# Performance work log

Hardware: AMD Instinct MI355X
Metric: run time of the kernel (lower is better)

## Reference

```python
import jax, jax.numpy as jnp
import numpy as np
from jax import lax

F32 = jnp.float32
EDT_ITERS = 16  # iterations for erosion-based distance transform approximation


def _maxpool(x, win):
    # x: (B, 1, D, H, W); stride-1 'SAME' max pool (pads with -inf like torch)
    return lax.reduce_window(x, -jnp.inf, lax.max, (1, 1) + win, (1, 1, 1, 1, 1), 'SAME')


def _minpool(x, win):
    return -_maxpool(-x, win)


def soft_erode(img):
    p1 = _minpool(img, (3, 1, 1))
    p2 = _minpool(img, (1, 3, 1))
    p3 = _minpool(img, (1, 1, 3))
    return jnp.minimum(jnp.minimum(p1, p2), p3)


def soft_dilate(img):
    return _maxpool(img, (3, 3, 3))


def soft_open(img):
    return soft_dilate(soft_erode(img))


def soft_skel(img, num_iter=10):
    # clDice soft skeletonization (SoftSkeletonize, num_iter=10)
    skel = jax.nn.relu(img - soft_open(img))
    for _ in range(num_iter):
        img = soft_erode(img)
        delta = jax.nn.relu(img - soft_open(img))
        skel = skel + jax.nn.relu(delta - skel * delta)
    return skel


def edt_approx(mask):
    # mask: (B, D, H, W) binary float. Distance-to-background via iterated
    # 3x3x3 erosion (chessboard metric approximation of distance_transform_edt).
    m = mask[:, None]

    def body(carry, _):
        cur, acc = carry
        acc = acc + cur
        cur = _minpool(cur, (3, 3, 3))
        return (cur, acc), None

    (_, acc), _ = lax.scan(body, (m, jnp.zeros_like(m)), None, length=EDT_ITERS)
    return acc[:, 0]


def get_weights(mask_input, skel_input, prob_flag):
    # dim == 3 path of the original get_weights, vectorized over batch
    if prob_flag:
        mask = (mask_input > 0.5).astype(F32)
        skel = (skel_input > 0.5).astype(F32)
    else:
        mask, skel = mask_input, skel_input
    dist = lax.stop_gradient(edt_approx(mask)) * mask
    skel_radius = dist * skel
    red = (1, 2, 3)
    rmax = jnp.maximum(jnp.max(skel_radius, axis=red, keepdims=True), 1.0)
    rmin = jnp.maximum(jnp.min(skel_radius, axis=red, keepdims=True), 1.0)
    dist_map_norm = jnp.minimum(dist, rmax) / rmax
    skel_R_norm = skel_radius / rmax
    I_norm = ((rmax - skel_radius + rmin) / rmax) ** 2 * skel  # dim == 3 -> squared
    if prob_flag:
        return dist_map_norm * mask_input, skel_R_norm * mask_input, I_norm * skel_input
    return dist_map_norm * mask, skel_R_norm * mask, I_norm * skel


def binary_fg_prob(net_output):
    # max over foreground channels, 2-way softmax, foreground probability
    fore = jnp.max(net_output[:, 1:], axis=1, keepdims=True)
    logits2 = jnp.concatenate([net_output[:, :1], fore], axis=1)
    return jax.nn.softmax(logits2, axis=1)[:, 1]  # (B, D, H, W)


def general_union(pred, tgt, weight):
    smooth, alpha, eps = 1.0, 0.1, 1e-4
    inter = jnp.sum(weight * (pred + eps) ** 0.7 * tgt)
    union = jnp.sum(weight * (alpha * pred + (1.0 - alpha) * tgt))
    return 1.0 - (inter + smooth) / (union + smooth)


def union_loss(net_output, target):
    prob = binary_fg_prob(net_output)
    y_true = (target[:, 0] > 0).astype(F32)
    hard = lax.stop_gradient((prob > 0.5).astype(F32))
    skel_pred_hard = lax.stop_gradient(soft_skel(hard[:, None], 10)[:, 0])
    skel_true = lax.stop_gradient(soft_skel(y_true[:, None], 10)[:, 0])
    skel_pred_prob = skel_pred_hard * prob
    q_vl, _, q_sl = get_weights(y_true, skel_true, prob_flag=False)
    q_vp, _, q_sp = get_weights(prob, skel_pred_prob, prob_flag=True)
    return general_union(q_sp, q_vl, q_sp) + general_union(q_vp, q_sl, q_sl)


def cldice_loss(net_output, target, num_iter=10, smooth=1.0):
    prob = binary_fg_prob(net_output)
    y_true = (target[:, 0] > 0).astype(F32)
    skel_pred = soft_skel(prob[:, None], num_iter)[:, 0]
    skel_true = soft_skel(y_true[:, None], num_iter)[:, 0]
    tprec = (jnp.sum(skel_pred * y_true) + smooth) / (jnp.sum(skel_pred) + smooth)
    tsens = (jnp.sum(skel_true * prob) + smooth) / (jnp.sum(skel_true) + smooth)
    return 1.0 - 2.0 * tprec * tsens / (tprec + tsens)


def soft_dice_loss(net_output, target, smooth=1e-5):
    # nnUNet SoftDiceLoss: softmax nonlin, batch_dice=True, do_bg=False
    pred = jax.nn.softmax(net_output, axis=1)
    C = net_output.shape[1]
    onehot = jnp.moveaxis(jax.nn.one_hot(target[:, 0], C, dtype=F32), -1, 1)
    axes = (0, 2, 3, 4)
    tp = jnp.sum(pred * onehot, axis=axes)
    fp = jnp.sum(pred * (1.0 - onehot), axis=axes)
    fn = jnp.sum((1.0 - pred) * onehot, axis=axes)
    dc = (2.0 * tp + smooth) / (2.0 * tp + fp + fn + smooth)
    return -jnp.mean(dc[1:])


def ce_loss(net_output, labels):
    logp = jax.nn.log_softmax(net_output, axis=1)
    nll = -jnp.take_along_axis(logp, labels[:, None], axis=1)[:, 0]
    return jnp.mean(nll)


def _sobel_kernels():
    sx = np.array([[-1, 0, 1], [-2, 0, 2], [-1, 0, 1]], np.float32)
    kx_t = np.stack([sx, sx, sx], axis=0)[None, None]  # (1,1,3,3,3) OIDHW
    ky_t = np.transpose(kx_t, (0, 1, 3, 2, 4))
    kz_t = np.transpose(kx_t, (0, 1, 4, 2, 3))

    def pred_k(k):  # (1,2,3,3,3): second input channel is all-zero like the torch kernel
        return np.concatenate([k, np.zeros_like(k)], axis=1)

    return (pred_k(kx_t), pred_k(ky_t), pred_k(kz_t)), (kx_t, ky_t, kz_t)


def _conv3d(x, k):
    return lax.conv_general_dilated(x, jnp.asarray(k), (1, 1, 1), 'SAME',
                                    dimension_numbers=('NCDHW', 'OIDHW', 'NCDHW'))


def directional_loss(pred, target):
    kp, kt = _sobel_kernels()
    gp = jnp.stack([_conv3d(pred, k) for k in kp], axis=-1)    # (B,1,D,H,W,3)
    gt = jnp.stack([_conv3d(target, k) for k in kt], axis=-1)  # (B,1,D,H,W,3)

    def normalize(v):
        n = jnp.linalg.norm(v, axis=-1, keepdims=True)
        return v / jnp.maximum(n, 1e-12)

    gpn, gtn = normalize(gp), normalize(gt)
    num = jnp.sum(gpn * gtn, axis=-1)
    den = jnp.maximum(jnp.linalg.norm(gpn, axis=-1) * jnp.linalg.norm(gtn, axis=-1), 1e-8)
    return 1.0 - jnp.mean(num / den)


def connectivity_loss(pred, target):
    pb = (pred > 0.5).astype(F32)
    tb = (target > 0.5).astype(F32)
    return jnp.mean(jnp.abs(pb - tb))  # broadcasts (B,2,...) against (B,1,...)


def combined_loss(net_output, target):
    tgt_f = target.astype(F32)
    labels = target[:, 0]
    return (soft_dice_loss(net_output, target)
            + ce_loss(net_output, labels)
            + cldice_loss(net_output, target)
            + directional_loss(net_output, tgt_f)
            + connectivity_loss(net_output, tgt_f)
            + union_loss(net_output, target))


def setup_inputs() -> dict:
    key = jax.random.key(0)
    k1, k2 = jax.random.split(key)
    net_output = jax.random.normal(k1, (2, 2, 64, 128, 128), dtype=jnp.float32)
    target = jax.random.randint(k2, (2, 1, 64, 128, 128), 0, 2, dtype=jnp.int32)
    return {'net_output': net_output, 'target': target, 't_skeletonize_flage': 0}


def reference(net_output, target, t_skeletonize_flage):
    # t_skeletonize_flage=0 -> soft (morphological) skeletonization path
    return combined_loss(net_output, target)
```

## Files before the change

kernel.cpp:

```cpp
#include <hip/hip_runtime.h>
#include <math.h>

typedef unsigned long long u64;
typedef unsigned int u32;
typedef unsigned short u16;
typedef unsigned char u8;

#define VOL 1048576
#define NTOT 2097152
#define NWORDS 32768
#define PC0 2048
#define PC1 2048

union HU { u16 u; _Float16 h; };
__device__ __forceinline__ float h2f(u16 u){ HU x; x.u=u; return (float)x.h; }
__device__ __forceinline__ u16 f2h(float f){ HU x; x.h=(_Float16)f; return x.u; }
#define H_ONE2 0x3C003C00u

__device__ __forceinline__ u32 pmin(u32 a, u32 b){ u32 r; asm("v_pk_min_f16 %0, %1, %2" : "=v"(r) : "v"(a), "v"(b)); return r; }
__device__ __forceinline__ u32 pmax(u32 a, u32 b){ u32 r; asm("v_pk_max_f16 %0, %1, %2" : "=v"(r) : "v"(a), "v"(b)); return r; }

__device__ __forceinline__ double wred(double v){
  #pragma unroll
  for(int o=32;o;o>>=1) v += __shfl_down(v, o);
  return v;
}

__device__ __forceinline__ u32 nib_compact(u64 v){
  v &= 0x0F0F0F0F0F0F0F0Full;
  v |= v>>4;  v &= 0x00FF00FF00FF00FFull;
  v |= v>>8;  v &= 0x0000FFFF0000FFFFull;
  v |= v>>16;
  return (u32)v;
}

__global__ __launch_bounds__(256) void k_init(const float* __restrict__ net, const int* __restrict__ tgt,
    u16* __restrict__ img, u16* __restrict__ prob, u64* __restrict__ ybits, u64* __restrict__ hbits,
    u64* __restrict__ bimg2, double* __restrict__ part)
{
  __shared__ u64 nyb[32], nhb[32];
  __shared__ double sw[5][4];
  int tid = threadIdx.x;
  int r = blockIdx.x*256 + tid;
  int n0 = r<<2;
  int b = n0>>20, v0 = n0&(VOL-1);
  const float* nb = net + (size_t)b*(2*VOL);
  float4 a0 = *(const float4*)&nb[v0];
  float4 a1 = *(const float4*)&nb[VOL+v0];
  int4  tv = *(const int4*)&tgt[n0];
  float x0a[4] = {a0.x,a0.y,a0.z,a0.w};
  float x1a[4] = {a1.x,a1.y,a1.z,a1.w};
  int   ta[4]  = {tv.x,tv.y,tv.z,tv.w};
  double ce=0,tp=0,spr=0,sy=0,conn=0;
  u32 pk[2] = {0,0};
  u32 y4=0, h4=0;
  #pragma unroll
  for(int e=0;e<4;e++){
    float d = x1a[e]-x0a[e];
    int yb = (ta[e]>0) ? 1 : 0;
    float p = 1.f/(1.f+__expf(-d));
    y4 |= (u32)yb<<e;
    h4 |= (u32)(d>0.f)<<e;
    pk[e>>1] |= (u32)f2h(p) << ((e&1)*16);
    ce += (double)(log1pf(__expf(-fabsf(d))) + fmaxf(yb? -d : d, 0.f));
    tp += (double)p*yb;
    spr += (double)p;
    sy += (double)yb;
    conn += (double)((int)((x0a[e]>0.5f)!=(yb!=0)) + (int)((x1a[e]>0.5f)!=(yb!=0)));
  }
  u32* f1 = (u32*)img;
  u32* f4 = (u32*)prob;
  int pi = r<<1;
  f1[pi] = pk[0]; f1[pi+1] = pk[1];
  f4[pi] = pk[0]; f4[pi+1] = pk[1];
  ((u8*)nyb)[tid] = (u8)y4;
  ((u8*)nhb)[tid] = (u8)h4;
  __syncthreads();
  if (tid < 16){
    u64 wy = (u64)nib_compact(nyb[tid*2]) | ((u64)nib_compact(nyb[tid*2+1])<<32);
    u64 wh = (u64)nib_compact(nhb[tid*2]) | ((u64)nib_compact(nhb[tid*2+1])<<32);
    int wi = blockIdx.x*16 + tid;
    ybits[wi]=wy; bimg2[wi]=wy;
    hbits[wi]=wh; bimg2[NWORDS+wi]=wh;
  }
  int wid = tid>>6, lane = tid&63;
  double vals[5] = {ce,tp,spr,sy,conn};
  #pragma unroll
  for(int s=0;s<5;s++){ double rr = wred(vals[s]); if(lane==0) sw[s][wid]=rr; }
  __syncthreads();
  if(tid==0){
    #pragma unroll
    for(int s=0;s<5;s++) part[(size_t)s*PC0 + blockIdx.x] = sw[s][0]+sw[s][1]+sw[s][2]+sw[s][3];
  }
}

template<bool INIT>
__global__ __launch_bounds__(256) void fskel2(const u16* __restrict__ imgin, u16* __restrict__ imgout,
                                              u16* __restrict__ skel)
{
  __shared__ u32 A_[2800];
  __shared__ u32 B_[1728];
  __shared__ u32 C_[1080];
  int bid = blockIdx.x;
  int xb = bid&3, yb=(bid>>2)&15, zb=(bid>>6)&15, b=bid>>10;
  int X0=xb*32, Y0=yb*8, Z0=zb*4;
  const u32* vin = (const u32*)(imgin + (size_t)b*VOL);
  u32* vout = (u32*)(imgout + (size_t)b*VOL);
  u32* skl = (u32*)(skel + (size_t)b*VOL);
  int tid = threadIdx.x;

  {
    int y0 = tid/20, x0 = tid - y0*20;
    int gy0 = Y0-3+y0, gx0 = X0-4+2*x0;
    bool ok0 = ((unsigned)gy0<128u) & ((unsigned)gx0<128u);
    int gb0 = (gy0<<6)+(gx0>>1);
    int t1 = tid+256; int y1 = t1/20, x1 = t1-y1*20;
    int gy1 = Y0-3+y1, gx1 = X0-4+2*x1;
    bool hv1 = tid<24;
    bool ok1 = ((unsigned)gy1<128u) & ((unsigned)gx1<128u);
    int gb1 = (gy1<<6)+(gx1>>1);
    #pragma unroll
    for(int z=0; z<10; ++z){
      int gz = Z0-3+z;
      bool zok = (unsigned)gz<64u;
      int zb2 = gz<<13;
      A_[z*280+tid] = (zok&ok0) ? vin[zb2+gb0] : H_ONE2;
      if (hv1) A_[z*280+t1] = (zok&ok1) ? vin[zb2+gb1] : H_ONE2;
    }
  }
  __syncthreads();
  if (tid < 216){
    int y = tid/18, px = tid - y*18;
    int gy = Y0-2+y;
    bool yok = (unsigned)gy<128u;
    bool xout = ((X0==0)&&(px==0)) || ((X0==96)&&(px==17));
    #pragma unroll
    for(int z=0; z<8; ++z){
      bool zok = (unsigned)(Z0-2+z)<64u;
      u32 v = H_ONE2;
      if (zok && yok && !xout){
        int c = (z+1)*280 + (y+1)*20 + (px+1);
        u32 C0=A_[c], L=A_[c-1], R=A_[c+1];
        u32 SL=(L>>16)|(C0<<16), SR=(C0>>16)|(R<<16);
        u32 m = pmin(pmin(SL,SR), C0);
        m = pmin(m, pmin(A_[c-20],A_[c+20]));
        v = pmin(m, pmin(A_[c-280],A_[c+280]));
      }
      B_[z*216+tid] = v;
    }
  }
  __syncthreads();
  if (tid < 180){
    int y = tid/18, px = tid - y*18;
    int gy = Y0-1+y;
    bool yok = (unsigned)gy<128u;
    bool xout = ((X0==0)&&(px==0)) || ((X0==96)&&(px==17));
    bool ctr = (px>=1)&&(px<=16)&&(y>=1)&&(y<=8);
    int pxm = (px>0)? px-1 : 0;
    int pxp = (px<17)? px+1 : 17;
    int gb = (gy<<6)+((X0-2+2*px)>>1);
    #pragma unroll
    for(int z=0; z<6; ++z){
      int gz = Z0-1+z;
      bool zok = (unsigned)gz<64u;
      u32 v = 0;
      if (zok && yok && !xout){
        int c = (z+1)*216 + (y+1)*18;
        u32 C0=B_[c+px], L=B_[c+pxm], R=B_[c+pxp];
        u32 SL=(L>>16)|(C0<<16), SR=(C0>>16)|(R<<16);
        u32 m = pmin(pmin(SL,SR), C0);
        m = pmin(m, pmin(B_[c+px-18],B_[c+px+18]));
        v = pmin(m, pmin(B_[c-216+px],B_[c+216+px]));
      }
      C_[z*180+tid] = v;
      if (ctr && z>=1 && z<=4)
        vout[(gz<<13)+gb] = v;
    }
  }
  int col = tid>>1, zh = tid&1;
  int oy = col>>4, opx = col&15;
  u32 ek0[2], ek1[2];
  #pragma unroll
  for(int j=0;j<2;j++){
    int z = zh*2+j;
    ek0[j] = A_[(z+3)*280+(oy+3)*20+(opx+2)];
    ek1[j] = B_[(z+2)*216+(oy+2)*18+(opx+1)];
  }
  __syncthreads();
  u32* X1 = A_; u32* X2 = A_ + 960;
  if (tid < 160){
    int y = tid>>4, px = tid&15;
    int px1 = px+1;
    int gy = Y0-1+y;
    bool yok = (unsigned)gy<128u;
    bool mlo = (X0==0)&&(px==0);
    bool mhi = (X0==96)&&(px==15);
    #pragma unroll
    for(int z=0; z<6; ++z){
      bool zok = (unsigned)(Z0-1+z)<64u;
      {
        int c = (z+1)*216 + (y+1)*18 + px1;
        u32 C0=B_[c], L=B_[c-1], R=B_[c+1];
        if (mlo) L = 0;
        if (mhi) R = 0;
        u32 SL=(L>>16)|(C0<<16), SR=(C0>>16)|(R<<16);
        u32 v = pmax(pmax(SL,SR), C0);
        X1[z*160+tid] = (zok&&yok) ? v : 0;
      }
      {
        int c = z*180 + y*18 + px1;
        u32 C0=C_[c], L=C_[c-1], R=C_[c+1];
        u32 SL=(L>>16)|(C0<<16), SR=(C0>>16)|(R<<16);
        X2[z*160+tid] = pmax(pmax(SL,SR), C0);
      }
    }
  }
  __syncthreads();
  u32* Y1 = B_; u32* Y2 = B_ + 768;
  {
    int arr = tid>>7, rem = tid&127;
    int y = rem>>4, px = rem&15;
    const u32* Xs = arr ? X2 : X1;
    u32* Ys = arr ? Y2 : Y1;
    #pragma unroll
    for(int z=0; z<6; ++z){
      int c = z*160 + y*16 + px;
      Ys[z*128 + rem] = pmax(pmax(Xs[c], Xs[c+16]), Xs[c+32]);
    }
  }
  __syncthreads();
  {
    int gx = X0 + 2*opx;
    #pragma unroll
    for(int j=0;j<2;j++){
      int z = zh*2+j;
      int gz = Z0+z;
      int c = z*128 + oy*16 + opx;
      u32 o1 = pmax(pmax(Y1[c], Y1[c+128]), Y1[c+256]);
      u32 o2 = pmax(pmax(Y2[c], Y2[c+128]), Y2[c+256]);
      u32 idx = (u32)((gz<<13) + ((Y0+oy)<<6) + (gx>>1));
      float d0l = fmaxf(h2f((u16)ek0[j]) - h2f((u16)o1), 0.f);
      float d0h = fmaxf(h2f((u16)(ek0[j]>>16)) - h2f((u16)(o1>>16)), 0.f);
      float d1l = fmaxf(h2f((u16)ek1[j]) - h2f((u16)o2), 0.f);
      float d1h = fmaxf(h2f((u16)(ek1[j]>>16)) - h2f((u16)(o2>>16)), 0.f);
      float sl_, sh_;
      if (INIT){ sl_ = d0l; sh_ = d0h; }
      else {
        u32 swv = skl[idx];
        sl_ = h2f((u16)swv); sh_ = h2f((u16)(swv>>16));
        sl_ += fmaxf(d0l - sl_*d0l, 0.f); sh_ += fmaxf(d0h - sh_*d0h, 0.f);
      }
      sl_ += fmaxf(d1l - sl_*d1l, 0.f); sh_ += fmaxf(d1h - sh_*d1h, 0.f);
      skl[idx] = (u32)f2h(sl_) | ((u32)f2h(sh_)<<16);
    }
  }
}

__global__ __launch_bounds__(256) void fskel1(const u16* __restrict__ imgin, u16* __restrict__ skel)
{
  __shared__ u32 A2[1920];
  __shared__ u32 B2[1080];
  int bid = blockIdx.x;
  int xb = bid&3, yb=(bid>>2)&15, zb=(bid>>6)&15, b=bid>>10;
  int X0=xb*32, Y0=yb*8, Z0=zb*4;
  const u32* vin = (const u32*)(imgin + (size_t)b*VOL);
  u32* skl = (u32*)(skel + (size_t)b*VOL);
  int tid = threadIdx.x;
  if (tid < 240){
    int y0 = tid/20, x0 = tid - y0*20;
    int gy0 = Y0-2+y0, gx0 = X0-4+2*x0;
    bool ok0 = ((unsigned)gy0<128u) & ((unsigned)gx0<128u);
    int gb0 = (gy0<<6)+(gx0>>1);
    #pragma unroll
    for(int z=0; z<8; ++z){
      int gz = Z0-2+z;
      bool zok = (unsigned)gz<64u;
      A2[z*240+tid] = (zok&ok0) ? vin[(gz<<13)+gb0] : H_ONE2;
    }
  }
  __syncthreads();
  if (tid < 180){
    int y = tid/18, px = tid - y*18;
    int gy = Y0-1+y;
    bool yok = (unsigned)gy<128u;
    bool xout = ((X0==0)&&(px==0)) || ((X0==96)&&(px==17));
    int pxm = (px>0)? px-1 : 0;
    int pxp = (px<17)? px+1 : 17;
    #pragma unroll
    for(int z=0; z<6; ++z){
      bool zok = (unsigned)(Z0-1+z)<64u;
      u32 v = 0;
      if (zok && yok && !xout){
        int c = (z+1)*240 + (y+1)*20;
        u32 C0=A2[c+px+1], L=A2[c+pxm+1], R=A2[c+pxp+1];
        u32 SL=(L>>16)|(C0<<16), SR=(C0>>16)|(R<<16);
        u32 m = pmin(pmin(SL,SR), C0);
        m = pmin(m, pmin(A2[c+px+1-20],A2[c+px+1+20]));
        v = pmin(m, pmin(A2[c-240+px+1],A2[c+240+px+1]));
      }
      B2[z*180+tid] = v;
    }
  }
  int col = tid>>1, zh = tid&1;
  int oy = col>>4, opx = col&15;
  u32 ek[2];
  #pragma unroll
  for(int j=0;j<2;j++){
    int z = zh*2+j;
    ek[j] = A2[(z+2)*240+(oy+2)*20+(opx+2)];
  }
  __syncthreads();
  u32* X = A2;
  if (tid < 160){
    int y = tid>>4, px = tid&15;
    int px1 = px+1;
    #pragma unroll
    for(int z=0; z<6; ++z){
      int c = z*180 + y*18 + px1;
      u32 C0=B2[c], L=B2[c-1], R=B2[c+1];
      u32 SL=(L>>16)|(C0<<16), SR=(C0>>16)|(R<<16);
      X[z*160+tid] = pmax(pmax(SL,SR), C0);
    }
  }
  __syncthreads();
  u32* Y = B2;
  if (tid < 128){
    int y = tid>>4, px = tid&15;
    #pragma unroll
    for(int z=0; z<6; ++z){
      int c = z*160 + y*16 + px;
      Y[z*128 + tid] = pmax(pmax(X[c], X[c+16]), X[c+32]);
    }
  }
  __syncthreads();
  {
    int gx = X0 + 2*opx;
    #pragma unroll
    for(int j=0;j<2;j++){
      int z = zh*2+j;
      int gz = Z0+z;
      int c = z*128 + oy*16 + opx;
      u32 o = pmax(pmax(Y[c], Y[c+128]), Y[c+256]);
      u32 idx = (u32)((gz<<13) + ((Y0+oy)<<6) + (gx>>1));
      float dl = fmaxf(h2f((u16)ek[j]) - h2f((u16)o), 0.f);
      float dh = fmaxf(h2f((u16)(ek[j]>>16)) - h2f((u16)(o>>16)), 0.f);
      u32 swv = skl[idx];
      float sl_ = h2f((u16)swv), sh_ = h2f((u16)(swv>>16));
      sl_ += fmaxf(dl - sl_*dl, 0.f); sh_ += fmaxf(dh - sh_*dh, 0.f);
      skl[idx] = (u32)f2h(sl_) | ((u32)f2h(sh_)<<16);
    }
  }
}

__device__ __forceinline__ u64 berode_x(const u64* P, int tid){
  u64 c = P[tid];
  if (tid & 1) return c & ((c<<1)|(P[tid-1]>>63)) & ((c>>1)|(1ull<<63));
  else         return c & ((c<<1)|1ull) & ((c>>1)|(P[tid+1]<<63));
}
__device__ __forceinline__ u64 bdilate_x(const u64* P, int tid){
  u64 c = P[tid];
  if (tid & 1) return c | (c<<1) | (P[tid-1]>>63) | (c>>1);
  else         return c | (c<<1) | (c>>1) | (P[tid+1]<<63);
}

template<bool INIT>
__global__ __launch_bounds__(256) void bskel(const u64* __restrict__ imgin, u64* __restrict__ imgout,
                                             u64* __restrict__ skel)
{
  __shared__ u64 simg[4][256];
  __shared__ u64 se1[6][256];
  __shared__ u64 se2[2][256];
  __shared__ u64 sM[4][256];
  int bid = blockIdx.x;
  int tzb = bid & 31, b = (bid>>5)&1, m = bid>>6;
  int z0 = tzb*2, z1 = z0+2;
  size_t base = (size_t)m*NWORDS + (size_t)b*16384;
  const u64* vin = imgin + base;
  u64* vout = imgout + base;
  u64* skl = skel + base;
  int tid = threadIdx.x;
  int y = tid>>1;

  for (int s = z0-3; s <= z1+6; ++s){
    if (s <= z1+2)
      simg[(s+96)&3][tid] = ((unsigned)s<64u) ? vin[(s<<8)+tid] : ~0ull;
    { int t = s-2;
      if (t >= z0-2 && t <= z1+1){
        u64 r = ~0ull;
        if ((unsigned)t<64u){
          const u64* P = simg[(t+96)&3];
          if (INIT) r = P[tid];
          else {
            r = berode_x(P, tid);
            if(y>0)   r &= P[tid-2];
            if(y<127) r &= P[tid+2];
            r &= simg[(t-1+96)&3][tid] & simg[(t+1+96)&3][tid];
          }
        }
        se1[(t+96)%6][tid] = r;
      }
    }
    { int t = s-4;
      if (t >= z0-1 && t <= z1){
        u64 r = 0;
        if ((unsigned)t<64u){
          const u64* P = se1[(t+96)%6];
          r = berode_x(P, tid);
          if(y>0)   r &= P[tid-2];
          if(y<127) r &= P[tid+2];
          r &= se1[(t-1+96)%6][tid] & se1[(t+1+96)%6][tid];
        }
        se2[(t+96)&1][tid] = r;
      }
    }
    { int t = s-5;
      if (t >= z0-1 && t <= z1){
        const u64* P = se2[(t+96)&1];
        u64 dm = bdilate_x(P, tid);
        if(y>0)   dm |= bdilate_x(P, tid-2);
        if(y<127) dm |= bdilate_x(P, tid+2);
        sM[(t+96)&3][tid] = dm;
      }
    }
    { int z = s-7;
      if (z >= z0 && z < z1){
        u64 open_ = sM[(z-1+96)&3][tid] | sM[(z+96)&3][tid] | sM[(z+1+96)&3][tid];
        u64 e1v = se1[(z+96)%6][tid];
        u64 d = e1v & ~open_;
        int gw = (z<<8)+tid;
        if (INIT) skl[gw] = d;
        else { skl[gw] |= d; vout[gw] = e1v; }
      }
    }
    __syncthreads();
  }
}

__global__ __launch_bounds__(256) void edt_px(const u64* __restrict__ yb, const u64* __restrict__ hb,
                                              u8* __restrict__ d)
{
  int g = blockIdx.x*256 + threadIdx.x;
  int m = g >> 21;
  int n = g & (NTOT-1);
  const u64* bits = m ? hb : yb;
  int x = n & 127;
  int row = n >> 7;
  u64 w0 = bits[row*2], w1 = bits[row*2+1];
  int a = x - 31;
  u64 win;
  if (a < 0)        win = w0 << (-a);
  else if (a == 0)  win = w0;
  else if (a < 64)  win = (w0 >> a) | (w1 << (64-a));
  else              win = w1 >> (a-64);
  if (x < 31)  win |= (1ull << (31-x)) - 1;
  if (x > 95)  win |= (~0ull) << (159-x);
  u64 inv = ~win;
  u64 tl = inv & 0xFFFFFFFFull;
  u64 tr = inv >> 31;
  int dl = tl ? (31 - (63 - __clzll(tl))) : 99;
  int dr = tr ? (__ffsll((unsigned long long)tr) - 1) : 99;
  d[(size_t)g] = (u8)min(min(dl, dr), 16);
}

__global__ __launch_bounds__(256) void edt_py(const u8* __restrict__ din, u8* __restrict__ dout){
  int g = blockIdx.x*256 + threadIdx.x;
  int n = g & (NTOT-1);
  int c = (n >> 7) & 127;
  size_t idx = (size_t)g;
  int best = din[idx];
  #pragma unroll 4
  for (int k=1; k<=16; ++k){
    if (best <= k) break;
    int v = 255;
    if (c-k >= 0)   v = din[idx - (size_t)k*128];
    if (c+k < 128)  v = min(v, (int)din[idx + (size_t)k*128]);
    best = min(best, max(k, v));
  }
  dout[idx] = (u8)best;
}

__global__ __launch_bounds__(256) void edt_pz_part(const u8* __restrict__ din, u8* __restrict__ dout,
    const u64* __restrict__ skel2, const u64* __restrict__ hbits,
    u8* __restrict__ pmaxv, u8* __restrict__ pminv)
{
  int tid = threadIdx.x;
  int g = blockIdx.x*256 + tid;
  int m = g >> 21;
  int n = g & (NTOT-1);
  int c = (n >> 14) & 63;
  size_t idx = (size_t)g;
  int best = din[idx];
  #pragma unroll 4
  for (int k=1; k<=16; ++k){
    if (best <= k) break;
    int v = 255;
    if (c-k >= 0)  v = din[idx - (size_t)k*16384];
    if (c+k < 64)  v = min(v, (int)din[idx + (size_t)k*16384]);
    best = min(best, max(k, v));
  }
  dout[idx] = (u8)best;
  int wi = n>>6, bit = n&63;
  u64 sbit = m ? (skel2[NWORDS+wi] & hbits[wi]) : skel2[wi];
  u32 r = (u32)((sbit>>bit)&1ull) ? (u32)best : 0u;
  __shared__ u32 sx[256], sn_[256];
  sx[tid]=r; sn_[tid]=r;
  __syncthreads();
  for(int s=128;s>0;s>>=1){
    if(tid<s){
      if(sx[tid+s]>sx[tid]) sx[tid]=sx[tid+s];
      if(sn_[tid+s]<sn_[tid]) sn_[tid]=sn_[tid+s];
    }
    __syncthreads();
  }
  if(tid==0){ pmaxv[blockIdx.x]=(u8)sx[0]; pminv[blockIdx.x]=(u8)sn_[0]; }
}

__global__ __launch_bounds__(256) void rmm2(const u8* __restrict__ pmaxv, const u8* __restrict__ pminv,
                                            u32* __restrict__ mm){
  __shared__ u8 smx[4][256], smn[4][256];
  int tid = threadIdx.x;
  u8 mx[4]={0,0,0,0}, mn[4]={255,255,255,255};
  for(int i=tid;i<16384;i+=256){
    int sel=i>>13, b=(i>>12)&1, cc=sel*2+b;
    u8 a=pmaxv[i], d=pminv[i];
    if(a>mx[cc]) mx[cc]=a;
    if(d<mn[cc]) mn[cc]=d;
  }
  #pragma unroll
  for(int cc=0;cc<4;cc++){ smx[cc][tid]=mx[cc]; smn[cc][tid]=mn[cc]; }
  __syncthreads();
  for(int s=128;s>0;s>>=1){
    if(tid<s){
      #pragma unroll
      for(int cc=0;cc<4;cc++){
        if(smx[cc][tid+s]>smx[cc][tid]) smx[cc][tid]=smx[cc][tid+s];
        if(smn[cc][tid+s]<smn[cc][tid]) smn[cc][tid]=smn[cc][tid+s];
      }
    }
    __syncthreads();
  }
  if(tid==0){
    #pragma unroll
    for(int cc=0;cc<4;cc++){
      int sel=cc>>1, b=cc&1;
      mm[sel*4+b]   = (u32)smx[cc][0];
      mm[sel*4+2+b] = (u32)smn[cc][0];
    }
  }
}

__global__ __launch_bounds__(256) void k_tail(const float* __restrict__ net, const u16* __restrict__ prob,
    const u16* __restrict__ skelp, const u64* __restrict__ ybits, const u64* __restrict__ hbits,
    const u64* __restrict__ skel2, const u8* __restrict__ acc, const u32* __restrict__ mm,
    double* __restrict__ part1)
{
  __shared__ float lp[2040];
  __shared__ float dxp[1920];
  __shared__ float sxp[1920];
  __shared__ char  dxt8[1920];
  __shared__ u8    sxt8[1920];
  __shared__ u64   wrow[60];
  __shared__ double sw[9][4];
  int tid = threadIdx.x;
  int bid = blockIdx.x;
  int xb = bid&3, ybk=(bid>>2)&15, zbk=(bid>>6)&15, b=bid>>10;
  int X0=xb*32, Y0=ybk*8, Z0=zbk*4;
  const float* P = net + (size_t)b*(2*VOL);
  float rmaxT = fmaxf((float)mm[b],1.f),   rminT = fmaxf((float)mm[2+b],1.f);
  float rmaxH = fmaxf((float)mm[4+b],1.f), rminH = fmaxf((float)mm[6+b],1.f);
  for (int idx=tid; idx<2040; idx+=256){
    int zr = idx/340; int rem = idx-zr*340; int yr = rem/34; int xi = rem-yr*34;
    int gz=Z0-1+zr, gy=Y0-1+yr, gx=X0-1+xi;
    float v = 0.f;
    if((unsigned)gz<64u && (unsigned)gy<128u && (unsigned)gx<128u)
      v = P[(gz<<14)+(gy<<7)+gx];
    lp[idx] = v;
  }
  if (tid < 60){
    int zr = tid/10, yr = tid-zr*10;
    int gz=Z0-1+zr, gy=Y0-1+yr;
    u64 wn = 0;
    if((unsigned)gz<64u && (unsigned)gy<128u){
      const u64* yw = ybits + ((size_t)b<<14) + (gz<<8) + (gy<<1);
      u64 w0 = yw[0], w1 = yw[1];
      if (X0==0) wn = w0<<1;
      else { int s = X0-1; wn = (s<64) ? ((w0>>s)|(w1<<(64-s))) : (w1>>(s-64)); }
    }
    wrow[tid] = wn;
  }
  __syncthreads();
  for (int idx=tid; idx<1920; idx+=256){
    int zr = idx/320; int rem = idx-zr*320; int yr = rem>>5; int x = rem&31;
    int c = zr*340 + yr*34 + x;
    float l0=lp[c], l1=lp[c+1], l2=lp[c+2];
    dxp[idx] = l2-l0;
    sxp[idx] = l0+2.f*l1+l2;
    u64 wn = wrow[zr*10+yr];
    int bm=(int)((wn>>x)&1ull), b1=(int)((wn>>(x+1))&1ull), bp=(int)((wn>>(x+2))&1ull);
    dxt8[idx] = (char)(bp-bm);
    sxt8[idx] = (u8)(bm+2*b1+bp);
  }
  __syncthreads();
  int oy = tid>>5, ox = tid&31;
  float A1[6],A2[6],A3[6];
  int   B1v[6],B2v[6],B3v[6];
  #pragma unroll
  for(int zr=0; zr<6; ++zr){
    int base = zr*320 + oy*32 + ox;
    float d0=dxp[base], d1=dxp[base+32], d2=dxp[base+64];
    A1[zr] = d0+2.f*d1+d2;
    A2[zr] = d0+d1+d2;
    float s0=sxp[base], s1=sxp[base+32], s2=sxp[base+64];
    A3[zr] = s0+s1+s2;
    int t0=dxt8[base], t1=dxt8[base+32], t2=dxt8[base+64];
    B1v[zr] = t0+2*t1+t2;
    B2v[zr] = t0+t1+t2;
    int u0=sxt8[base], u1=sxt8[base+32], u2=sxt8[base+64];
    B3v[zr] = u0+u1+u2;
  }
  double fsob=0,cl1=0,cl2=0,cl3=0,cl4=0,i1=0,un1=0,i2=0,un2=0;
  #pragma unroll
  for(int zc=0; zc<4; ++zc){
    float gpx = A1[zc]+A1[zc+1]+A1[zc+2];
    float gpy = A2[zc]+2.f*A2[zc+1]+A2[zc+2];
    float gpz = A3[zc+2]-A3[zc];
    float ftx = (float)(B1v[zc]+B1v[zc+1]+B1v[zc+2]);
    float fty = (float)(B2v[zc]+2*B2v[zc+1]+B2v[zc+2]);
    float ftz = (float)(B3v[zc+2]-B3v[zc]);
    float s1 = gpx*gpx+gpy*gpy+gpz*gpz;
    float s2 = ftx*ftx+fty*fty+ftz*ftz;
    if (s1>0.f && s2>0.f){
      float ip = rsqrtf(s1), it = rsqrtf(s2);
      fsob += (double)((gpx*ftx+gpy*fty+gpz*ftz)*ip*it);
    }
    int gz=Z0+zc, gy=Y0+oy, gx=X0+ox;
    int n = (b<<20)+(gz<<14)+(gy<<7)+gx;
    int yb = (int)((wrow[(zc+1)*10+(oy+1)] >> (ox+1)) & 1ull);
    int wi = n>>6, bit = n&63;
    int hd = (int)((hbits[wi]>>bit)&1ull);
    int sT = (int)((skel2[wi]>>bit)&1ull);
    int sH = (int)((skel2[NWORDS+wi]>>bit)&1ull);
    float dT = (float)acc[n];
    float dH = (float)acc[(size_t)NTOT+n];
    float p  = h2f(prob[n]);
    float sk = h2f(skelp[n]);
    cl1 += (double)(sk*(float)yb);
    cl2 += (double)sk;
    float q_vl = yb ? fminf(dT,rmaxT)/rmaxT : 0.f;
    if (sT){
      cl3 += (double)p; cl4 += 1.0;
      float t=(rmaxT-dT+rminT)/rmaxT; float q_sl=t*t;
      float q_vp = fminf(dH,rmaxH)/rmaxH*p;
      i2  += (double)(q_sl*__powf(q_vp+1e-4f,0.7f)*q_sl);
      un2 += (double)(q_sl*(0.1f*q_vp+0.9f*q_sl));
    }
    if (sH & hd){
      float t=(rmaxH-dH+rminH)/rmaxH; float q_sp=t*t*p;
      i1  += (double)(q_sp*__powf(q_sp+1e-4f,0.7f)*q_vl);
      un1 += (double)(q_sp*(0.1f*q_sp+0.9f*q_vl));
    }
  }
  int wid = tid>>6, lane = tid&63;
  double vals[9] = {fsob,cl1,cl2,cl3,cl4,i1,un1,i2,un2};
  #pragma unroll
  for(int s=0;s<9;s++){ double rr = wred(vals[s]); if(lane==0) sw[s][wid]=rr; }
  __syncthreads();
  if(tid==0){
    #pragma unroll
    for(int s=0;s<9;s++) part1[(size_t)s*PC1 + bid] = sw[s][0]+sw[s][1]+sw[s][2]+sw[s][3];
  }
}

__global__ __launch_bounds__(256) void k_reduce_mid(const double* __restrict__ part0,
                                                    const double* __restrict__ part1,
                                                    double* __restrict__ tot){
  int s = blockIdx.x;
  const double* src; int n;
  if (s < 5){ src = part0 + (size_t)s*PC0; n = PC0; }
  else      { src = part1 + (size_t)(s-5)*PC1; n = PC1; }
  double v=0;
  for(int i=threadIdx.x;i<n;i+=256) v += src[i];
  __shared__ double sd[256];
  sd[threadIdx.x]=v; __syncthreads();
  for(int k=128;k>0;k>>=1){ if((int)threadIdx.x<k) sd[threadIdx.x]+=sd[threadIdx.x+k]; __syncthreads(); }
  if(threadIdx.x==0) tot[s]=sd[0];
}

__global__ void k_fin(const double* __restrict__ tot, float* __restrict__ out){
  if(threadIdx.x==0 && blockIdx.x==0){
    const double N = (double)NTOT;
    double ce = tot[0]/N;
    double tp=tot[1], fp=tot[2]-tot[1], fn=tot[3]-tot[1];
    double dice = -((2.0*tp+1e-5)/(2.0*tp+fp+fn+1e-5));
    double conn = tot[4]/(2.0*N);
    double dir  = 1.0 - tot[5]/N;
    double tprec = (tot[6]+1.0)/(tot[7]+1.0);
    double tsens = (tot[8]+1.0)/(tot[9]+1.0);
    double cld = 1.0 - 2.0*tprec*tsens/(tprec+tsens);
    double u1 = 1.0 - (tot[10]+1.0)/(tot[11]+1.0);
    double u2 = 1.0 - (tot[12]+1.0)/(tot[13]+1.0);
    out[0] = (float)(dice+ce+cld+dir+conn+u1+u2);
  }
}

extern "C" void kernel_launch(void* const* d_in, const int* in_sizes, int n_in,
                              void* d_out, int out_size, void* d_ws, size_t ws_size,
                              hipStream_t stream)
{
  (void)in_sizes; (void)n_in; (void)out_size; (void)ws_size;
  const float* net = (const float*)d_in[0];
  const int*   tgt = (const int*)d_in[1];
  float* out = (float*)d_out;
  char* w = (char*)d_ws;
  const size_t MB = 1024*1024;
  u16* F1 = (u16*)(w + 0*MB);
  u16* F2 = (u16*)(w + 4*MB);
  u16* F3 = (u16*)(w + 8*MB);
  u16* F4 = (u16*)(w + 12*MB);
  u64* ybits = (u64*)(w + 16*MB);
  u64* hbits = ybits + NWORDS;
  u64* skel2 = hbits + NWORDS;
  u64* bping = skel2 + 2*NWORDS;
  u64* bpong = bping + 2*NWORDS;
  u8*  dA    = (u8*)(bpong + 2*NWORDS);
  u8*  dB    = dA + (size_t)2*NTOT;
  double* part0 = (double*)(dB + (size_t)2*NTOT);
  double* part1 = part0 + (size_t)5*PC0;
  double* tot   = part1 + (size_t)9*PC1;
  u8* pmaxv = (u8*)(tot + 16);
  u8* pminv = pmaxv + 16384;
  u32* mm  = (u32*)(pminv + 16384);

  k_init<<<PC0, 256, 0, stream>>>(net, tgt, F1, F4, ybits, hbits, bping, part0);

  bskel<true><<<128,256,0,stream>>>(bping, bpong, skel2);
  {
    u64* pi=bping; u64* po=bpong;
    for(int i=0;i<10;i++){ bskel<false><<<128,256,0,stream>>>(pi,po,skel2); u64* t=pi; pi=po; po=t; }
  }

  fskel2<true><<<2048,256,0,stream>>>(F1, F3, F2);
  fskel2<false><<<2048,256,0,stream>>>(F3, F1, F2);
  fskel2<false><<<2048,256,0,stream>>>(F1, F3, F2);
  fskel2<false><<<2048,256,0,stream>>>(F3, F1, F2);
  fskel2<false><<<2048,256,0,stream>>>(F1, F3, F2);
  fskel1<<<2048,256,0,stream>>>(F3, F2);

  const int GE = (2*NTOT)/256;
  edt_px<<<GE,256,0,stream>>>(ybits, hbits, dA);
  edt_py<<<GE,256,0,stream>>>(dA, dB);
  edt_pz_part<<<GE,256,0,stream>>>(dB, dA, skel2, hbits, pmaxv, pminv);
  rmm2<<<1,256,0,stream>>>(pmaxv, pminv, mm);

  k_tail<<<PC1,256,0,stream>>>(net, F4, F2, ybits, hbits, skel2, dA, mm, part1);
  k_reduce_mid<<<14,256,0,stream>>>(part0, part1, tot);
  k_fin<<<1,64,0,stream>>>(tot, out);
}
```

Measured before the change: 321.5 us.

## Fuse EDT x-pass into init, atomic min/max, and enlarge skeleton tiles

```diff
diff --git a/kernel.cpp b/kernel.cpp
--- a/kernel.cpp
+++ b/kernel.cpp
@@ -34,13 +34,33 @@
   return (u32)v;
 }
 
+__device__ __forceinline__ int edt_x1(u64 w0, u64 w1, int x){
+  int a = x-31;
+  u64 win;
+  if (a<0)        win = w0 << (-a);
+  else if (a==0)  win = w0;
+  else if (a<64)  win = (w0>>a)|(w1<<(64-a));
+  else            win = w1>>(a-64);
+  if (x<31) win |= (1ull<<(31-x))-1;
+  if (x>95) win |= (~0ull)<<(159-x);
+  u64 inv = ~win;
+  u64 tl = inv & 0xFFFFFFFFull;
+  u64 tr = inv>>31;
+  int dl = tl ? (31-(63-__clzll(tl))) : 99;
+  int dr = tr ? (__ffsll((unsigned long long)tr)-1) : 99;
+  return min(min(dl,dr),16);
+}
+
 __global__ __launch_bounds__(256) void k_init(const float* __restrict__ net, const int* __restrict__ tgt,
     u16* __restrict__ img, u16* __restrict__ prob, u64* __restrict__ ybits, u64* __restrict__ hbits,
-    u64* __restrict__ bimg2, double* __restrict__ part)
+    u64* __restrict__ bimg2, u8* __restrict__ dA, u32* __restrict__ mm, double* __restrict__ part)
 {
   __shared__ u64 nyb[32], nhb[32];
+  __shared__ u64 swy[16], swh[16];
   __shared__ double sw[5][4];
   int tid = threadIdx.x;
+  if (blockIdx.x==0 && tid<8)
+    mm[tid] = (tid==2||tid==3||tid==6||tid==7) ? 0xFFFFFFFFu : 0u;
   int r = blockIdx.x*256 + tid;
   int n0 = r<<2;
   int b = n0>>20, v0 = n0&(VOL-1);
@@ -82,6 +102,24 @@
     int wi = blockIdx.x*16 + tid;
     ybits[wi]=wy; bimg2[wi]=wy;
     hbits[wi]=wh; bimg2[NWORDS+wi]=wh;
+    swy[tid]=wy; swh[tid]=wh;
+  }
+  __syncthreads();
+  {
+    int ln = tid<<2;
+    int row = ln>>7;
+    int xq = ln&127;
+    int gn0 = blockIdx.x*1024 + ln;
+    u64 wy0 = swy[row*2], wy1 = swy[row*2+1];
+    u64 wh0 = swh[row*2], wh1 = swh[row*2+1];
+    u32 oy4=0, oh4=0;
+    #pragma unroll
+    for(int e=0;e<4;e++){
+      oy4 |= (u32)edt_x1(wy0,wy1,xq+e) << (8*e);
+      oh4 |= (u32)edt_x1(wh0,wh1,xq+e) << (8*e);
+    }
+    *(u32*)&dA[gn0] = oy4;
+    *(u32*)&dA[(size_t)NTOT+gn0] = oh4;
   }
   int wid = tid>>6, lane = tid&63;
   double vals[5] = {ce,tp,spr,sy,conn};
@@ -95,145 +133,113 @@
 }
 
 template<bool INIT>
-__global__ __launch_bounds__(256) void fskel2(const u16* __restrict__ imgin, u16* __restrict__ imgout,
+__global__ __launch_bounds__(512) void fskel2(const u16* __restrict__ imgin, u16* __restrict__ imgout,
                                               u16* __restrict__ skel)
 {
-  __shared__ u32 A_[2800];
-  __shared__ u32 B_[1728];
-  __shared__ u32 C_[1080];
+  __shared__ u32 A_[3920];
+  __shared__ u32 B_[2592];
+  __shared__ u32 C_[1800];
   int bid = blockIdx.x;
-  int xb = bid&3, yb=(bid>>2)&15, zb=(bid>>6)&15, b=bid>>10;
-  int X0=xb*32, Y0=yb*8, Z0=zb*4;
+  int xb = bid&3, yb=(bid>>2)&15, zb=(bid>>6)&7, b=bid>>9;
+  int X0=xb*32, Y0=yb*8, Z0=zb*8;
   const u32* vin = (const u32*)(imgin + (size_t)b*VOL);
   u32* vout = (u32*)(imgout + (size_t)b*VOL);
   u32* skl = (u32*)(skel + (size_t)b*VOL);
   int tid = threadIdx.x;
 
-  {
-    int y0 = tid/20, x0 = tid - y0*20;
-    int gy0 = Y0-3+y0, gx0 = X0-4+2*x0;
-    bool ok0 = ((unsigned)gy0<128u) & ((unsigned)gx0<128u);
-    int gb0 = (gy0<<6)+(gx0>>1);
-    int t1 = tid+256; int y1 = t1/20, x1 = t1-y1*20;
-    int gy1 = Y0-3+y1, gx1 = X0-4+2*x1;
-    bool hv1 = tid<24;
-    bool ok1 = ((unsigned)gy1<128u) & ((unsigned)gx1<128u);
-    int gb1 = (gy1<<6)+(gx1>>1);
-    #pragma unroll
-    for(int z=0; z<10; ++z){
-      int gz = Z0-3+z;
-      bool zok = (unsigned)gz<64u;
-      int zb2 = gz<<13;
-      A_[z*280+tid] = (zok&ok0) ? vin[zb2+gb0] : H_ONE2;
-      if (hv1) A_[z*280+t1] = (zok&ok1) ? vin[zb2+gb1] : H_ONE2;
-    }
-  }
-  __syncthreads();
-  if (tid < 216){
-    int y = tid/18, px = tid - y*18;
-    int gy = Y0-2+y;
-    bool yok = (unsigned)gy<128u;
+  for (int idx=tid; idx<3920; idx+=512){
+    int z = idx/280; int rem = idx - z*280; int y = rem/20; int px = rem - y*20;
+    int gz = Z0-3+z, gy = Y0-3+y, gx = X0-4+2*px;
+    bool ok = ((unsigned)gz<64u) & ((unsigned)gy<128u) & ((unsigned)gx<128u);
+    A_[idx] = ok ? vin[(gz<<13)+(gy<<6)+(gx>>1)] : H_ONE2;
+  }
+  __syncthreads();
+  for (int idx=tid; idx<2592; idx+=512){
+    int z = idx/216; int rem = idx - z*216; int y = rem/18; int px = rem - y*18;
+    int gz = Z0-2+z, gy = Y0-2+y;
+    bool zok = (unsigned)gz<64u, yok = (unsigned)gy<128u;
     bool xout = ((X0==0)&&(px==0)) || ((X0==96)&&(px==17));
-    #pragma unroll
-    for(int z=0; z<8; ++z){
-      bool zok = (unsigned)(Z0-2+z)<64u;
-      u32 v = H_ONE2;
-      if (zok && yok && !xout){
-        int c = (z+1)*280 + (y+1)*20 + (px+1);
-        u32 C0=A_[c], L=A_[c-1], R=A_[c+1];
-        u32 SL=(L>>16)|(C0<<16), SR=(C0>>16)|(R<<16);
-        u32 m = pmin(pmin(SL,SR), C0);
-        m = pmin(m, pmin(A_[c-20],A_[c+20]));
-        v = pmin(m, pmin(A_[c-280],A_[c+280]));
-      }
-      B_[z*216+tid] = v;
-    }
-  }
-  __syncthreads();
-  if (tid < 180){
-    int y = tid/18, px = tid - y*18;
-    int gy = Y0-1+y;
-    bool yok = (unsigned)gy<128u;
+    u32 v = H_ONE2;
+    if (zok && yok && !xout){
+      int c = (z+1)*280 + (y+1)*20 + (px+1);
+      u32 C0=A_[c], L=A_[c-1], R=A_[c+1];
+      u32 SL=(L>>16)|(C0<<16), SR=(C0>>16)|(R<<16);
+      u32 m = pmin(pmin(SL,SR), C0);
+      m = pmin(m, pmin(A_[c-20],A_[c+20]));
+      v = pmin(m, pmin(A_[c-280],A_[c+280]));
+    }
+    B_[idx] = v;
+  }
+  __syncthreads();
+  for (int idx=tid; idx<1800; idx+=512){
+    int z = idx/180; int rem = idx - z*180; int y = rem/18; int px = rem - y*18;
+    int gz = Z0-1+z, gy = Y0-1+y;
+    bool zok=(unsigned)gz<64u, yok=(unsigned)gy<128u;
     bool xout = ((X0==0)&&(px==0)) || ((X0==96)&&(px==17));
-    bool ctr = (px>=1)&&(px<=16)&&(y>=1)&&(y<=8);
-    int pxm = (px>0)? px-1 : 0;
-    int pxp = (px<17)? px+1 : 17;
-    int gb = (gy<<6)+((X0-2+2*px)>>1);
-    #pragma unroll
-    for(int z=0; z<6; ++z){
-      int gz = Z0-1+z;
-      bool zok = (unsigned)gz<64u;
-      u32 v = 0;
-      if (zok && yok && !xout){
-        int c = (z+1)*216 + (y+1)*18;
-        u32 C0=B_[c+px], L=B_[c+pxm], R=B_[c+pxp];
-        u32 SL=(L>>16)|(C0<<16), SR=(C0>>16)|(R<<16);
-        u32 m = pmin(pmin(SL,SR), C0);
-        m = pmin(m, pmin(B_[c+px-18],B_[c+px+18]));
-        v = pmin(m, pmin(B_[c-216+px],B_[c+216+px]));
-      }
-      C_[z*180+tid] = v;
-      if (ctr && z>=1 && z<=4)
-        vout[(gz<<13)+gb] = v;
-    }
-  }
-  int col = tid>>1, zh = tid&1;
-  int oy = col>>4, opx = col&15;
+    int pxm = (px>0)?px-1:0, pxp=(px<17)?px+1:17;
+    u32 v = 0;
+    if (zok && yok && !xout){
+      int c = (z+1)*216 + (y+1)*18;
+      u32 C0=B_[c+px], L=B_[c+pxm], R=B_[c+pxp];
+      u32 SL=(L>>16)|(C0<<16), SR=(C0>>16)|(R<<16);
+      u32 m = pmin(pmin(SL,SR), C0);
+      m = pmin(m, pmin(B_[c+px-18],B_[c+px+18]));
+      v = pmin(m, pmin(B_[c-216+px],B_[c+216+px]));
+    }
+    C_[idx] = v;
+    if (px>=1 && px<=16 && y>=1 && y<=8 && z>=1 && z<=8)
+      vout[(gz<<13)+(gy<<6)+((X0-2+2*px)>>1)] = v;
+  }
+  int zq = tid>>7, cc = tid&127;
+  int oy = cc>>4, opx = cc&15;
   u32 ek0[2], ek1[2];
   #pragma unroll
   for(int j=0;j<2;j++){
-    int z = zh*2+j;
-    ek0[j] = A_[(z+3)*280+(oy+3)*20+(opx+2)];
-    ek1[j] = B_[(z+2)*216+(oy+2)*18+(opx+1)];
-  }
-  __syncthreads();
-  u32* X1 = A_; u32* X2 = A_ + 960;
-  if (tid < 160){
-    int y = tid>>4, px = tid&15;
-    int px1 = px+1;
-    int gy = Y0-1+y;
-    bool yok = (unsigned)gy<128u;
-    bool mlo = (X0==0)&&(px==0);
-    bool mhi = (X0==96)&&(px==15);
-    #pragma unroll
-    for(int z=0; z<6; ++z){
-      bool zok = (unsigned)(Z0-1+z)<64u;
-      {
-        int c = (z+1)*216 + (y+1)*18 + px1;
-        u32 C0=B_[c], L=B_[c-1], R=B_[c+1];
-        if (mlo) L = 0;
-        if (mhi) R = 0;
-        u32 SL=(L>>16)|(C0<<16), SR=(C0>>16)|(R<<16);
-        u32 v = pmax(pmax(SL,SR), C0);
-        X1[z*160+tid] = (zok&&yok) ? v : 0;
-      }
-      {
-        int c = z*180 + y*18 + px1;
-        u32 C0=C_[c], L=C_[c-1], R=C_[c+1];
-        u32 SL=(L>>16)|(C0<<16), SR=(C0>>16)|(R<<16);
-        X2[z*160+tid] = pmax(pmax(SL,SR), C0);
-      }
-    }
-  }
-  __syncthreads();
-  u32* Y1 = B_; u32* Y2 = B_ + 768;
-  {
-    int arr = tid>>7, rem = tid&127;
-    int y = rem>>4, px = rem&15;
+    int z = zq*2+j;
+    ek0[j] = A_[(z+3)*280 + (oy+3)*20 + (opx+2)];
+    ek1[j] = B_[(z+2)*216 + (oy+2)*18 + (opx+1)];
+  }
+  __syncthreads();
+  u32* X1 = A_; u32* X2 = A_ + 1600;
+  for (int idx=tid; idx<3200; idx+=512){
+    int arr = (idx>=1600);
+    int r2 = arr ? idx-1600 : idx;
+    int z = r2/160; int rem = r2 - z*160; int y = rem>>4; int px = rem&15;
+    u32 v;
+    if (!arr){
+      int gz = Z0-1+z, gy = Y0-1+y;
+      bool ok = ((unsigned)gz<64u) && ((unsigned)gy<128u);
+      int c = (z+1)*216 + (y+1)*18 + (px+1);
+      u32 C0=B_[c], L=B_[c-1], R=B_[c+1];
+      if ((X0==0)&&(px==0)) L=0;
+      if ((X0==96)&&(px==15)) R=0;
+      u32 SL=(L>>16)|(C0<<16), SR=(C0>>16)|(R<<16);
+      v = pmax(pmax(SL,SR), C0);
+      if (!ok) v = 0;
+    } else {
+      int c = z*180 + y*18 + (px+1);
+      u32 C0=C_[c], L=C_[c-1], R=C_[c+1];
+      u32 SL=(L>>16)|(C0<<16), SR=(C0>>16)|(R<<16);
+      v = pmax(pmax(SL,SR), C0);
+    }
+    A_[idx] = v;
+  }
+  __syncthreads();
+  for (int idx=tid; idx<2560; idx+=512){
+    int arr = (idx>=1280);
+    int r2 = arr ? idx-1280 : idx;
+    int z = r2>>7; int rem = r2&127; int y = rem>>4; int px = rem&15;
     const u32* Xs = arr ? X2 : X1;
-    u32* Ys = arr ? Y2 : Y1;
-    #pragma unroll
-    for(int z=0; z<6; ++z){
-      int c = z*160 + y*16 + px;
-      Ys[z*128 + rem] = pmax(pmax(Xs[c], Xs[c+16]), Xs[c+32]);
-    }
-  }
-  __syncthreads();
+    int c = z*160 + y*16 + px;
+    B_[idx] = pmax(pmax(Xs[c], Xs[c+16]), Xs[c+32]);
+  }
+  __syncthreads();
+  u32* Y1 = B_; u32* Y2 = B_ + 1280;
   {
     int gx = X0 + 2*opx;
     #pragma unroll
     for(int j=0;j<2;j++){
-      int z = zh*2+j;
+      int z = zq*2+j;
       int gz = Z0+z;
       int c = z*128 + oy*16 + opx;
       u32 o1 = pmax(pmax(Y1[c], Y1[c+128]), Y1[c+256]);
@@ -256,88 +262,70 @@
   }
 }
 
-__global__ __launch_bounds__(256) void fskel1(const u16* __restrict__ imgin, u16* __restrict__ skel)
+__global__ __launch_bounds__(512) void fskel1(const u16* __restrict__ imgin, u16* __restrict__ skel)
 {
-  __shared__ u32 A2[1920];
-  __shared__ u32 B2[1080];
+  __shared__ u32 A2[2880];
+  __shared__ u32 B2[1800];
   int bid = blockIdx.x;
-  int xb = bid&3, yb=(bid>>2)&15, zb=(bid>>6)&15, b=bid>>10;
-  int X0=xb*32, Y0=yb*8, Z0=zb*4;
+  int xb = bid&3, yb=(bid>>2)&15, zb=(bid>>6)&7, b=bid>>9;
+  int X0=xb*32, Y0=yb*8, Z0=zb*8;
   const u32* vin = (const u32*)(imgin + (size_t)b*VOL);
   u32* skl = (u32*)(skel + (size_t)b*VOL);
   int tid = threadIdx.x;
-  if (tid < 240){
-    int y0 = tid/20, x0 = tid - y0*20;
-    int gy0 = Y0-2+y0, gx0 = X0-4+2*x0;
-    bool ok0 = ((unsigned)gy0<128u) & ((unsigned)gx0<128u);
-    int gb0 = (gy0<<6)+(gx0>>1);
-    #pragma unroll
-    for(int z=0; z<8; ++z){
-      int gz = Z0-2+z;
-      bool zok = (unsigned)gz<64u;
-      A2[z*240+tid] = (zok&ok0) ? vin[(gz<<13)+gb0] : H_ONE2;
-    }
-  }
-  __syncthreads();
-  if (tid < 180){
-    int y = tid/18, px = tid - y*18;
-    int gy = Y0-1+y;
-    bool yok = (unsigned)gy<128u;
+  for (int idx=tid; idx<2880; idx+=512){
+    int z = idx/240; int rem = idx - z*240; int y = rem/20; int px = rem - y*20;
+    int gz = Z0-2+z, gy = Y0-2+y, gx = X0-4+2*px;
+    bool ok = ((unsigned)gz<64u) & ((unsigned)gy<128u) & ((unsigned)gx<128u);
+    A2[idx] = ok ? vin[(gz<<13)+(gy<<6)+(gx>>1)] : H_ONE2;
+  }
+  __syncthreads();
+  for (int idx=tid; idx<1800; idx+=512){
+    int z = idx/180; int rem = idx - z*180; int y = rem/18; int px = rem - y*18;
+    int gz = Z0-1+z, gy = Y0-1+y;
+    bool zok=(unsigned)gz<64u, yok=(unsigned)gy<128u;
     bool xout = ((X0==0)&&(px==0)) || ((X0==96)&&(px==17));
-    int pxm = (px>0)? px-1 : 0;
-    int pxp = (px<17)? px+1 : 17;
-    #pragma unroll
-    for(int z=0; z<6; ++z){
-      bool zok = (unsigned)(Z0-1+z)<64u;
-      u32 v = 0;
-      if (zok && yok && !xout){
-        int c = (z+1)*240 + (y+1)*20;
-        u32 C0=A2[c+px+1], L=A2[c+pxm+1], R=A2[c+pxp+1];
-        u32 SL=(L>>16)|(C0<<16), SR=(C0>>16)|(R<<16);
-        u32 m = pmin(pmin(SL,SR), C0);
-        m = pmin(m, pmin(A2[c+px+1-20],A2[c+px+1+20]));
-        v = pmin(m, pmin(A2[c-240+px+1],A2[c+240+px+1]));
-      }
-      B2[z*180+tid] = v;
-    }
-  }
-  int col = tid>>1, zh = tid&1;
-  int oy = col>>4, opx = col&15;
+    int pxm = (px>0)?px-1:0, pxp=(px<17)?px+1:17;
+    u32 v = 0;
+    if (zok && yok && !xout){
+      int c = (z+1)*240 + (y+1)*20;
+      u32 C0=A2[c+px+1], L=A2[c+pxm+1], R=A2[c+pxp+1];
+      u32 SL=(L>>16)|(C0<<16), SR=(C0>>16)|(R<<16);
+      u32 m = pmin(pmin(SL,SR), C0);
+      m = pmin(m, pmin(A2[c+px+1-20],A2[c+px+1+20]));
+      v = pmin(m, pmin(A2[c-240+px+1],A2[c+240+px+1]));
+    }
+    B2[idx] = v;
+  }
+  int zq = tid>>7, cc = tid&127;
+  int oy = cc>>4, opx = cc&15;
   u32 ek[2];
   #pragma unroll
   for(int j=0;j<2;j++){
-    int z = zh*2+j;
-    ek[j] = A2[(z+2)*240+(oy+2)*20+(opx+2)];
+    int z = zq*2+j;
+    ek[j] = A2[(z+2)*240 + (oy+2)*20 + (opx+2)];
   }
   __syncthreads();
   u32* X = A2;
-  if (tid < 160){
-    int y = tid>>4, px = tid&15;
-    int px1 = px+1;
-    #pragma unroll
-    for(int z=0; z<6; ++z){
-      int c = z*180 + y*18 + px1;
-      u32 C0=B2[c], L=B2[c-1], R=B2[c+1];
-      u32 SL=(L>>16)|(C0<<16), SR=(C0>>16)|(R<<16);
-      X[z*160+tid] = pmax(pmax(SL,SR), C0);
-    }
+  for (int idx=tid; idx<1600; idx+=512){
+    int z = idx/160; int rem = idx - z*160; int y = rem>>4; int px = rem&15;
+    int c = z*180 + y*18 + (px+1);
+    u32 C0=B2[c], L=B2[c-1], R=B2[c+1];
+    u32 SL=(L>>16)|(C0<<16), SR=(C0>>16)|(R<<16);
+    A2[idx] = pmax(pmax(SL,SR), C0);
   }
   __syncthreads();
   u32* Y = B2;
-  if (tid < 128){
-    int y = tid>>4, px = tid&15;
-    #pragma unroll
-    for(int z=0; z<6; ++z){
-      int c = z*160 + y*16 + px;
-      Y[z*128 + tid] = pmax(pmax(X[c], X[c+16]), X[c+32]);
-    }
+  for (int idx=tid; idx<1280; idx+=512){
+    int z = idx>>7; int rem = idx&127; int y = rem>>4; int px = rem&15;
+    int c = z*160 + y*16 + px;
+    B2[idx] = pmax(pmax(X[c], X[c+16]), X[c+32]);
   }
   __syncthreads();
   {
     int gx = X0 + 2*opx;
     #pragma unroll
     for(int j=0;j<2;j++){
-      int z = zh*2+j;
+      int z = zq*2+j;
       int gz = Z0+z;
       int c = z*128 + oy*16 + opx;
       u32 o = pmax(pmax(Y[c], Y[c+128]), Y[c+256]);
@@ -436,32 +424,6 @@
   }
 }
 
-__global__ __launch_bounds__(256) void edt_px(const u64* __restrict__ yb, const u64* __restrict__ hb,
-                                              u8* __restrict__ d)
-{
-  int g = blockIdx.x*256 + threadIdx.x;
-  int m = g >> 21;
-  int n = g & (NTOT-1);
-  const u64* bits = m ? hb : yb;
-  int x = n & 127;
-  int row = n >> 7;
-  u64 w0 = bits[row*2], w1 = bits[row*2+1];
-  int a = x - 31;
-  u64 win;
-  if (a < 0)        win = w0 << (-a);
-  else if (a == 0)  win = w0;
-  else if (a < 64)  win = (w0 >> a) | (w1 << (64-a));
-  else              win = w1 >> (a-64);
-  if (x < 31)  win |= (1ull << (31-x)) - 1;
-  if (x > 95)  win |= (~0ull) << (159-x);
-  u64 inv = ~win;
-  u64 tl = inv & 0xFFFFFFFFull;
-  u64 tr = inv >> 31;
-  int dl = tl ? (31 - (63 - __clzll(tl))) : 99;
-  int dr = tr ? (__ffsll((unsigned long long)tr) - 1) : 99;
-  d[(size_t)g] = (u8)min(min(dl, dr), 16);
-}
-
 __global__ __launch_bounds__(256) void edt_py(const u8* __restrict__ din, u8* __restrict__ dout){
   int g = blockIdx.x*256 + threadIdx.x;
   int n = g & (NTOT-1);
@@ -479,9 +441,8 @@
   dout[idx] = (u8)best;
 }
 
-__global__ __launch_bounds__(256) void edt_pz_part(const u8* __restrict__ din, u8* __restrict__ dout,
-    const u64* __restrict__ skel2, const u64* __restrict__ hbits,
-    u8* __restrict__ pmaxv, u8* __restrict__ pminv)
+__global__ __launch_bounds__(256) void edt_pz(const u8* __restrict__ din, u8* __restrict__ dout,
+    const u64* __restrict__ skel2, const u64* __restrict__ hbits, u32* __restrict__ mm)
 {
   int tid = threadIdx.x;
   int g = blockIdx.x*256 + tid;
@@ -512,40 +473,10 @@
     }
     __syncthreads();
   }
-  if(tid==0){ pmaxv[blockIdx.x]=(u8)sx[0]; pminv[blockIdx.x]=(u8)sn_[0]; }
-}
-
-__global__ __launch_bounds__(256) void rmm2(const u8* __restrict__ pmaxv, const u8* __restrict__ pminv,
-                                            u32* __restrict__ mm){
-  __shared__ u8 smx[4][256], smn[4][256];
-  int tid = threadIdx.x;
-  u8 mx[4]={0,0,0,0}, mn[4]={255,255,255,255};
-  for(int i=tid;i<16384;i+=256){
-    int sel=i>>13, b=(i>>12)&1, cc=sel*2+b;
-    u8 a=pmaxv[i], d=pminv[i];
-    if(a>mx[cc]) mx[cc]=a;
-    if(d<mn[cc]) mn[cc]=d;
-  }
-  #pragma unroll
-  for(int cc=0;cc<4;cc++){ smx[cc][tid]=mx[cc]; smn[cc][tid]=mn[cc]; }
-  __syncthreads();
-  for(int s=128;s>0;s>>=1){
-    if(tid<s){
-      #pragma unroll
-      for(int cc=0;cc<4;cc++){
-        if(smx[cc][tid+s]>smx[cc][tid]) smx[cc][tid]=smx[cc][tid+s];
-        if(smn[cc][tid+s]<smn[cc][tid]) smn[cc][tid]=smn[cc][tid+s];
-      }
-    }
-    __syncthreads();
-  }
   if(tid==0){
-    #pragma unroll
-    for(int cc=0;cc<4;cc++){
-      int sel=cc>>1, b=cc&1;
-      mm[sel*4+b]   = (u32)smx[cc][0];
-      mm[sel*4+2+b] = (u32)smn[cc][0];
-    }
+    int bb = (n>>20)&1;
+    atomicMax(&mm[m*4+bb], sx[0]);
+    atomicMin(&mm[m*4+2+bb], sn_[0]);
   }
 }
 
@@ -727,11 +658,9 @@
   double* part0 = (double*)(dB + (size_t)2*NTOT);
   double* part1 = part0 + (size_t)5*PC0;
   double* tot   = part1 + (size_t)9*PC1;
-  u8* pmaxv = (u8*)(tot + 16);
-  u8* pminv = pmaxv + 16384;
-  u32* mm  = (u32*)(pminv + 16384);
-
-  k_init<<<PC0, 256, 0, stream>>>(net, tgt, F1, F4, ybits, hbits, bping, part0);
+  u32* mm  = (u32*)(tot + 16);
+
+  k_init<<<PC0, 256, 0, stream>>>(net, tgt, F1, F4, ybits, hbits, bping, dA, mm, part0);
 
   bskel<true><<<128,256,0,stream>>>(bping, bpong, skel2);
   {
@@ -739,18 +668,16 @@
     for(int i=0;i<10;i++){ bskel<false><<<128,256,0,stream>>>(pi,po,skel2); u64* t=pi; pi=po; po=t; }
   }
 
-  fskel2<true><<<2048,256,0,stream>>>(F1, F3, F2);
-  fskel2<false><<<2048,256,0,stream>>>(F3, F1, F2);
-  fskel2<false><<<2048,256,0,stream>>>(F1, F3, F2);
-  fskel2<false><<<2048,256,0,stream>>>(F3, F1, F2);
-  fskel2<false><<<2048,256,0,stream>>>(F1, F3, F2);
-  fskel1<<<2048,256,0,stream>>>(F3, F2);
+  fskel2<true><<<1024,512,0,stream>>>(F1, F3, F2);
+  fskel2<false><<<1024,512,0,stream>>>(F3, F1, F2);
+  fskel2<false><<<1024,512,0,stream>>>(F1, F3, F2);
+  fskel2<false><<<1024,512,0,stream>>>(F3, F1, F2);
+  fskel2<false><<<1024,512,0,stream>>>(F1, F3, F2);
+  fskel1<<<1024,512,0,stream>>>(F3, F2);
 
   const int GE = (2*NTOT)/256;
-  edt_px<<<GE,256,0,stream>>>(ybits, hbits, dA);
   edt_py<<<GE,256,0,stream>>>(dA, dB);
-  edt_pz_part<<<GE,256,0,stream>>>(dB, dA, skel2, hbits, pmaxv, pminv);
-  rmm2<<<1,256,0,stream>>>(pmaxv, pminv, mm);
+  edt_pz<<<GE,256,0,stream>>>(dB, dA, skel2, hbits, mm);
 
   k_tail<<<PC1,256,0,stream>>>(net, F4, F2, ybits, hbits, skel2, dA, mm, part1);
   k_reduce_mid<<<14,256,0,stream>>>(part0, part1, tot);
```

Result: slower. 639.5 us (+98.9%).
